# Kernel optimization log

Hardware: AMD Instinct MI355X
Metric: run time of the kernel (lower is better)

## Reference

```python
import jax, jax.numpy as jnp
import numpy as np


def _topk_masked_softmax(attn, k):
    # Keep only the top-k entries per row (last dim), softmax over them.
    _, idx = jax.lax.top_k(attn, k)  # [b, nh, C, k]
    mask = jnp.put_along_axis(
        jnp.zeros(attn.shape, dtype=bool), idx, True, axis=-1, inplace=False
    )
    return jax.nn.softmax(jnp.where(mask, attn, -jnp.inf), axis=-1)


def setup_inputs() -> dict:
    key = jax.random.key(0)
    k0, k1, k2, k3, k4 = jax.random.split(key, 5)
    b, nh, C = 8, 8, 512
    attn = jax.random.normal(k0, (b, nh, C, C), dtype=jnp.float32)
    # In the torch module these are Parameters initialized to 0.2; use random
    # positive scalars of similar scale for a non-degenerate baseline.
    w1 = jax.random.uniform(k1, (1,), dtype=jnp.float32)
    w2 = jax.random.uniform(k2, (1,), dtype=jnp.float32)
    w3 = jax.random.uniform(k3, (1,), dtype=jnp.float32)
    w4 = jax.random.uniform(k4, (1,), dtype=jnp.float32)
    return {"attn": attn, "w1": w1, "w2": w2, "w3": w3, "w4": w4}


def reference(attn, w1, w2, w3, w4):
    C = attn.shape[-1]
    a1 = _topk_masked_softmax(attn, int(C / 2))
    a2 = _topk_masked_softmax(attn, int(C * 2 / 3))
    a3 = _topk_masked_softmax(attn, int(C * 3 / 4))
    a4 = _topk_masked_softmax(attn, int(C * 4 / 5))
    return a1 * w1 + a2 * w2 + a3 * w3 + a4 * w4
```

## Files before the change

kernel.cpp:

```cpp
#include <hip/hip_runtime.h>
#include <math.h>

#define ROW_C 512
#define NBIN 2048
#define NPACK (NBIN / 2)

__global__ __launch_bounds__(256) void topk_ms_kernel(
    const float* __restrict__ attn,
    const float* __restrict__ w1p, const float* __restrict__ w2p,
    const float* __restrict__ w3p, const float* __restrict__ w4p,
    float* __restrict__ out)
{
    __shared__ __align__(16) unsigned hist_all[4][NPACK];

    const int lane = threadIdx.x & 63;
    const int wv   = threadIdx.x >> 6;
    unsigned* h = hist_all[wv];
    int4* hv = (int4*)h;

    const long long row  = (long long)blockIdx.x * 4 + wv;
    const long long base = row * ROW_C + lane * 8;

    const float4 A = *reinterpret_cast<const float4*>(attn + base);
    const float4 B = *reinterpret_cast<const float4*>(attn + base + 4);
    const float orig[8] = {A.x, A.y, A.z, A.w, B.x, B.y, B.z, B.w};

    unsigned key[8];
    int bin[8];
    float eo[8];
    #pragma unroll
    for (int s = 0; s < 8; ++s) {
        const unsigned u = __float_as_uint(orig[s]);
        key[s] = (u & 0x80000000u) ? ~u : (u | 0x80000000u);
        const float y = fminf(fmaxf(orig[s], -3.90625f), 3.90625f) + 12.0f;
        bin[s] = (int)((__float_as_uint(y) >> 12) & 0x7FFu);
        eo[s] = __expf(orig[s]);
    }

    {
        const int4 z = make_int4(0, 0, 0, 0);
        hv[lane] = z; hv[lane + 64] = z; hv[lane + 128] = z; hv[lane + 192] = z;
    }

    #pragma unroll
    for (int s = 0; s < 8; ++s) {
        const int j  = bin[s] >> 1;
        const int ph = j ^ ((j >> 3) & 0x1C);
        atomicAdd(&h[ph], (bin[s] & 1) ? 0x10000u : 1u);
    }

    unsigned ps = 0;
    #pragma unroll
    for (int k = 0; k < 4; ++k) {
        const int b  = 4 * lane + k;
        const int pb = b ^ ((b >> 3) & 7);
        const int4 v = hv[pb];
        ps += (unsigned)v.x + (unsigned)v.y + (unsigned)v.z + (unsigned)v.w;
    }
    const unsigned tot = (ps & 0xFFFFu) + (ps >> 16);

    unsigned incl = tot;
    #pragma unroll
    for (int off = 1; off < 64; off <<= 1) {
        const unsigned t = __shfl_up(incl, off, 64);
        if (lane >= off) incl += t;
    }
    const unsigned excl = incl - tot;

    const unsigned long long Ba = __ballot(incl >= 257u);
    const unsigned long long Bb = __ballot(incl >= 172u);
    const unsigned long long Bc = __ballot(incl >= 129u);
    const unsigned long long Bd = __ballot(incl >= 104u);
    const int l0 = __ffsll(Ba) - 1, l1 = __ffsll(Bb) - 1,
              l2 = __ffsll(Bc) - 1, l3 = __ffsll(Bd) - 1;

    const int lsel = (lane == 0) ? l0 : (lane == 1) ? l1 : (lane == 2) ? l2 : l3;
    const int Tr   = (lane == 0) ? 257 : (lane == 1) ? 172 : (lane == 2) ? 129 : 104;
    const int Kr   = (lane == 0) ? 256 : (lane == 1) ? 341 : (lane == 2) ? 384 : 409;
    const unsigned exl = __shfl(excl, lsel & 63, 64);

    unsigned brR = 0u;
    if (lane < 4) {
        const int Tl = Tr - (int)exl;
        const unsigned T16 = (unsigned)Tl << 16;
        const int jbase = lsel << 4;
        const int xr = ((lsel >> 1) & 7) << 2;
        unsigned w[16];
        #pragma unroll
        for (int q = 0; q < 4; ++q) {
            const int pw = ((jbase + (q << 2)) ^ xr) >> 2;
            const int4 v = hv[pw];
            w[4*q+0] = (unsigned)v.x; w[4*q+1] = (unsigned)v.y;
            w[4*q+2] = (unsigned)v.z; w[4*q+3] = (unsigned)v.w;
        }
        unsigned run = 0, pcap = 0, rcap = 0; int jcap = 0; bool found = false;
        #pragma unroll
        for (int j = 0; j < 16; ++j) {
            const unsigned p = (w[j] + (w[j] << 16)) + (run + (run << 16));
            const bool ge   = (p >= T16);
            const bool take = ge && !found;
            pcap = take ? p   : pcap;
            rcap = take ? run : rcap;
            jcap = take ? j   : jcap;
            found = found || ge;
            run = p >> 16;
        }
        const int  lo   = (int)(pcap & 0xFFFFu);
        const bool ev   = (lo >= Tl);
        const int  bsel = (lsel << 5) + (jcap << 1) + (ev ? 0 : 1);
        const int  locp = ev ? lo : (int)(pcap >> 16);
        const int  prvp = ev ? (int)rcap : lo;
        const int  R    = Kr - 512 + (int)exl + locp;
        const unsigned allin = (prvp == Tl - 1) ? 1u : 0u;
        brR = ((unsigned)bsel << 17) | (allin << 16) | (unsigned)R;
    }

    int br_[4], Rr_[4], al_[4];
    #pragma unroll
    for (int r = 0; r < 4; ++r) {
        const unsigned v = __shfl(brR, r, 64);
        br_[r] = (int)(v >> 17);
        al_[r] = (int)((v >> 16) & 1u);
        Rr_[r] = (int)(v & 0xFFFFu);
    }

    unsigned tk[4]; int need[4], cnteq[4];
    #pragma unroll
    for (int r = 0; r < 4; ++r) {
        tk[r] = 0u; need[r] = 0; cnteq[r] = 0;
        if (!al_[r]) {
            unsigned cm[8];
            #pragma unroll
            for (int s = 0; s < 8; ++s)
                cm[s] = (bin[s] == br_[r]) ? key[s] : 0u;
            int R = Rr_[r];
            unsigned t; int c;
            while (true) {
                unsigned mk = cm[0];
                #pragma unroll
                for (int s = 1; s < 8; ++s) mk = (cm[s] > mk) ? cm[s] : mk;
                #pragma unroll
                for (int off = 32; off >= 1; off >>= 1) {
                    const unsigned o = __shfl_xor(mk, off, 64);
                    mk = (o > mk) ? o : mk;
                }
                t = mk;
                c = 0;
                #pragma unroll
                for (int s = 0; s < 8; ++s)
                    c += (int)__popcll(__ballot(cm[s] == t));
                if (c >= R) break;
                R -= c;
                #pragma unroll
                for (int s = 0; s < 8; ++s)
                    if (cm[s] == t) cm[s] = 0u;
            }
            tk[r] = t; need[r] = R; cnteq[r] = c;
        }
    }

    int fl[8] = {0, 0, 0, 0, 0, 0, 0, 0};
    #pragma unroll
    for (int r = 0; r < 4; ++r) {
        if (al_[r]) {
            const int bb = br_[r];
            #pragma unroll
            for (int s = 0; s < 8; ++s)
                fl[s] |= ((int)(bin[s] >= bb)) << r;
        } else if (need[r] == cnteq[r]) {
            const unsigned t = tk[r];
            #pragma unroll
            for (int s = 0; s < 8; ++s)
                fl[s] |= ((int)(key[s] >= t)) << r;
        } else {
            const unsigned t = tk[r];
            const unsigned long long ltm = (1ull << lane) - 1ull;
            int basec = 0;
            #pragma unroll
            for (int s = 0; s < 8; ++s)
                basec += (int)__popcll(__ballot(key[s] == t) & ltm);
            int own = 0;
            #pragma unroll
            for (int s = 0; s < 8; ++s) {
                const bool eq = (key[s] == t);
                if (key[s] > t || (eq && (basec + own) < need[r]))
                    fl[s] |= (1 << r);
                own += eq ? 1 : 0;
            }
        }
    }

    float z0 = 0.f, z1 = 0.f, z2 = 0.f, z3 = 0.f;
    #pragma unroll
    for (int s = 0; s < 8; ++s) {
        z0 += (fl[s] & 1) ? eo[s] : 0.f;
        z1 += (fl[s] & 2) ? eo[s] : 0.f;
        z2 += (fl[s] & 4) ? eo[s] : 0.f;
        z3 += (fl[s] & 8) ? eo[s] : 0.f;
    }
    #pragma unroll
    for (int off = 32; off >= 1; off >>= 1) {
        z0 += __shfl_xor(z0, off, 64);
        z1 += __shfl_xor(z1, off, 64);
        z2 += __shfl_xor(z2, off, 64);
        z3 += __shfl_xor(z3, off, 64);
    }

    const float wz0 = w1p[0] * __builtin_amdgcn_rcpf(z0);
    const float wz1 = w2p[0] * __builtin_amdgcn_rcpf(z1);
    const float wz2 = w3p[0] * __builtin_amdgcn_rcpf(z2);
    const float wz3 = w4p[0] * __builtin_amdgcn_rcpf(z3);

    float res[8];
    #pragma unroll
    for (int s = 0; s < 8; ++s) {
        float c = 0.f;
        c += (fl[s] & 1) ? wz0 : 0.f;
        c += (fl[s] & 2) ? wz1 : 0.f;
        c += (fl[s] & 4) ? wz2 : 0.f;
        c += (fl[s] & 8) ? wz3 : 0.f;
        res[s] = eo[s] * c;
    }
    *reinterpret_cast<float4*>(out + base)     = make_float4(res[0], res[1], res[2], res[3]);
    *reinterpret_cast<float4*>(out + base + 4) = make_float4(res[4], res[5], res[6], res[7]);
}

extern "C" void kernel_launch(void* const* d_in, const int* in_sizes, int n_in,
                              void* d_out, int out_size, void* d_ws, size_t ws_size,
                              hipStream_t stream) {
    const float* attn = (const float*)d_in[0];
    const float* w1   = (const float*)d_in[1];
    const float* w2   = (const float*)d_in[2];
    const float* w3   = (const float*)d_in[3];
    const float* w4   = (const float*)d_in[4];
    float* out = (float*)d_out;

    int rows = in_sizes[0] / ROW_C;
    int blocks = (rows + 3) / 4;
    topk_ms_kernel<<<blocks, 256, 0, stream>>>(attn, w1, w2, w3, w4, out);
}
```

Before: 136.4 us.

## Parallelize fine-bin search across 16-lane groups and compare floats directly

The bin-level search for each of the four top-k thresholds now runs on 16 lanes per threshold with a shuffle prefix scan, instead of one lane doing a serial 16-word scan. The sortable-integer keys are dropped in favour of comparing float values directly, and clamping uses fmed3. A fast path is added for the common case with no ties at a threshold: membership becomes four nested float comparisons with precomputed cumulative weights instead of building and decoding bit flags. This cuts serial latency and VALU work per wave, at the cost of more code and a divergent branch.

```diff
diff --git a/kernel.cpp b/kernel.cpp
--- a/kernel.cpp
+++ b/kernel.cpp
@@ -23,18 +23,15 @@
 
     const float4 A = *reinterpret_cast<const float4*>(attn + base);
     const float4 B = *reinterpret_cast<const float4*>(attn + base + 4);
-    const float orig[8] = {A.x, A.y, A.z, A.w, B.x, B.y, B.z, B.w};
-
-    unsigned key[8];
+    float x[8] = {A.x, A.y, A.z, A.w, B.x, B.y, B.z, B.w};
+
     int bin[8];
     float eo[8];
     #pragma unroll
     for (int s = 0; s < 8; ++s) {
-        const unsigned u = __float_as_uint(orig[s]);
-        key[s] = (u & 0x80000000u) ? ~u : (u | 0x80000000u);
-        const float y = fminf(fmaxf(orig[s], -3.90625f), 3.90625f) + 12.0f;
+        const float y = __builtin_amdgcn_fmed3f(x[s], -3.90625f, 3.90625f) + 12.0f;
         bin[s] = (int)((__float_as_uint(y) >> 12) & 0x7FFu);
-        eo[s] = __expf(orig[s]);
+        eo[s] = __expf(x[s]);
     }
 
     {
@@ -63,7 +60,7 @@
     #pragma unroll
     for (int off = 1; off < 64; off <<= 1) {
         const unsigned t = __shfl_up(incl, off, 64);
-        if (lane >= off) incl += t;
+        incl += (lane >= off) ? t : 0u;
     }
     const unsigned excl = incl - tot;
 
@@ -74,76 +71,72 @@
     const int l0 = __ffsll(Ba) - 1, l1 = __ffsll(Bb) - 1,
               l2 = __ffsll(Bc) - 1, l3 = __ffsll(Bd) - 1;
 
-    const int lsel = (lane == 0) ? l0 : (lane == 1) ? l1 : (lane == 2) ? l2 : l3;
-    const int Tr   = (lane == 0) ? 257 : (lane == 1) ? 172 : (lane == 2) ? 129 : 104;
-    const int Kr   = (lane == 0) ? 256 : (lane == 1) ? 341 : (lane == 2) ? 384 : 409;
-    const unsigned exl = __shfl(excl, lsel & 63, 64);
-
-    unsigned brR = 0u;
-    if (lane < 4) {
-        const int Tl = Tr - (int)exl;
-        const unsigned T16 = (unsigned)Tl << 16;
-        const int jbase = lsel << 4;
-        const int xr = ((lsel >> 1) & 7) << 2;
-        unsigned w[16];
-        #pragma unroll
-        for (int q = 0; q < 4; ++q) {
-            const int pw = ((jbase + (q << 2)) ^ xr) >> 2;
-            const int4 v = hv[pw];
-            w[4*q+0] = (unsigned)v.x; w[4*q+1] = (unsigned)v.y;
-            w[4*q+2] = (unsigned)v.z; w[4*q+3] = (unsigned)v.w;
-        }
-        unsigned run = 0, pcap = 0, rcap = 0; int jcap = 0; bool found = false;
-        #pragma unroll
-        for (int j = 0; j < 16; ++j) {
-            const unsigned p = (w[j] + (w[j] << 16)) + (run + (run << 16));
-            const bool ge   = (p >= T16);
-            const bool take = ge && !found;
-            pcap = take ? p   : pcap;
-            rcap = take ? run : rcap;
-            jcap = take ? j   : jcap;
-            found = found || ge;
-            run = p >> 16;
-        }
-        const int  lo   = (int)(pcap & 0xFFFFu);
-        const bool ev   = (lo >= Tl);
-        const int  bsel = (lsel << 5) + (jcap << 1) + (ev ? 0 : 1);
-        const int  locp = ev ? lo : (int)(pcap >> 16);
-        const int  prvp = ev ? (int)rcap : lo;
-        const int  R    = Kr - 512 + (int)exl + locp;
-        const unsigned allin = (prvp == Tl - 1) ? 1u : 0u;
-        brR = ((unsigned)bsel << 17) | (allin << 16) | (unsigned)R;
-    }
-
-    int br_[4], Rr_[4], al_[4];
-    #pragma unroll
-    for (int r = 0; r < 4; ++r) {
-        const unsigned v = __shfl(brR, r, 64);
-        br_[r] = (int)(v >> 17);
-        al_[r] = (int)((v >> 16) & 1u);
-        Rr_[r] = (int)(v & 0xFFFFu);
-    }
-
-    unsigned tk[4]; int need[4], cnteq[4];
-    #pragma unroll
-    for (int r = 0; r < 4; ++r) {
-        tk[r] = 0u; need[r] = 0; cnteq[r] = 0;
-        if (!al_[r]) {
-            unsigned cm[8];
+    const int r = lane >> 4;
+    const int i = lane & 15;
+    const int lsel = (r == 0) ? l0 : (r == 1) ? l1 : (r == 2) ? l2 : l3;
+    const int Tr   = (r == 0) ? 257 : (r == 1) ? 172 : (r == 2) ? 129 : 104;
+    const int Kr   = (r == 0) ? 256 : (r == 1) ? 341 : (r == 2) ? 384 : 409;
+    const unsigned exl = __shfl(excl, lsel, 64);
+
+    const int jw = (lsel << 4) + i;
+    const int pw = jw ^ ((jw >> 3) & 0x1C);
+    const unsigned w0 = h[pw];
+    const unsigned q  = w0 + (w0 << 16);
+    const unsigned wt = q >> 16;
+    unsigned sc = wt;
+    #pragma unroll
+    for (int off = 1; off < 16; off <<= 1) {
+        const unsigned t = __shfl_up(sc, off, 64);
+        sc += (i >= off) ? t : 0u;
+    }
+    const unsigned ebase = exl + (sc - wt);
+    const int      phi   = (int)(ebase + wt);
+    const unsigned long long CB = __ballot(phi >= Tr);
+    const int js = __ffs((unsigned)(CB >> (r << 4))) - 1;
+    const unsigned q_w  = __shfl(q, (r << 4) + js, 64);
+    const unsigned eb_w = __shfl(ebase, (r << 4) + js, 64);
+
+    const int  plo  = (int)(eb_w + (q_w & 0xFFFFu));
+    const int  phw  = (int)(eb_w + (q_w >> 16));
+    const bool ev   = (plo >= Tr);
+    const int  bsel = (((lsel << 4) + js) << 1) + (ev ? 0 : 1);
+    const int  locp = ev ? plo : phw;
+    const int  prvp = ev ? (int)eb_w : plo;
+    const int  Rr   = Kr - 512 + locp;
+    const int  alin = (prvp == Tr - 1) ? 1 : 0;
+    float tje = __uint_as_float((unsigned)(bsel + 0x41000) << 12) - 12.0f;
+    tje = (bsel <= 24) ? -__builtin_inff() : tje;
+    const unsigned pk = ((unsigned)bsel << 11) | ((unsigned)alin << 10) | (unsigned)Rr;
+
+    int b_[4], R_[4], al_[4]; float tthr[4];
+    #pragma unroll
+    for (int rr = 0; rr < 4; ++rr) {
+        const unsigned v = __shfl(pk, rr << 4, 64);
+        tthr[rr] = __shfl(tje, rr << 4, 64);
+        b_[rr]  = (int)(v >> 11);
+        al_[rr] = (int)((v >> 10) & 1u);
+        R_[rr]  = (int)(v & 0x3FFu);
+    }
+
+    int needv[4] = {0,0,0,0}, cntv[4] = {0,0,0,0};
+    bool anytb = false;
+    const float NINF = -__builtin_inff();
+    #pragma unroll
+    for (int rr = 0; rr < 4; ++rr) {
+        if (!al_[rr]) {
+            float cm[8];
             #pragma unroll
             for (int s = 0; s < 8; ++s)
-                cm[s] = (bin[s] == br_[r]) ? key[s] : 0u;
-            int R = Rr_[r];
-            unsigned t; int c;
+                cm[s] = (bin[s] == b_[rr]) ? x[s] : NINF;
+            int R = R_[rr];
+            float t; int c;
             while (true) {
-                unsigned mk = cm[0];
-                #pragma unroll
-                for (int s = 1; s < 8; ++s) mk = (cm[s] > mk) ? cm[s] : mk;
-                #pragma unroll
-                for (int off = 32; off >= 1; off >>= 1) {
-                    const unsigned o = __shfl_xor(mk, off, 64);
-                    mk = (o > mk) ? o : mk;
-                }
+                float mk = cm[0];
+                #pragma unroll
+                for (int s = 1; s < 8; ++s) mk = fmaxf(mk, cm[s]);
+                #pragma unroll
+                for (int off = 32; off >= 1; off >>= 1)
+                    mk = fmaxf(mk, __shfl_xor(mk, off, 64));
                 t = mk;
                 c = 0;
                 #pragma unroll
@@ -153,74 +146,99 @@
                 R -= c;
                 #pragma unroll
                 for (int s = 0; s < 8; ++s)
-                    if (cm[s] == t) cm[s] = 0u;
+                    cm[s] = (cm[s] == t) ? NINF : cm[s];
             }
-            tk[r] = t; need[r] = R; cnteq[r] = c;
-        }
-    }
-
-    int fl[8] = {0, 0, 0, 0, 0, 0, 0, 0};
-    #pragma unroll
-    for (int r = 0; r < 4; ++r) {
-        if (al_[r]) {
-            const int bb = br_[r];
-            #pragma unroll
-            for (int s = 0; s < 8; ++s)
-                fl[s] |= ((int)(bin[s] >= bb)) << r;
-        } else if (need[r] == cnteq[r]) {
-            const unsigned t = tk[r];
-            #pragma unroll
-            for (int s = 0; s < 8; ++s)
-                fl[s] |= ((int)(key[s] >= t)) << r;
-        } else {
-            const unsigned t = tk[r];
-            const unsigned long long ltm = (1ull << lane) - 1ull;
-            int basec = 0;
-            #pragma unroll
-            for (int s = 0; s < 8; ++s)
-                basec += (int)__popcll(__ballot(key[s] == t) & ltm);
-            int own = 0;
-            #pragma unroll
-            for (int s = 0; s < 8; ++s) {
-                const bool eq = (key[s] == t);
-                if (key[s] > t || (eq && (basec + own) < need[r]))
-                    fl[s] |= (1 << r);
-                own += eq ? 1 : 0;
+            tthr[rr] = t; needv[rr] = R; cntv[rr] = c;
+            anytb = anytb || (c != R);
+        }
+    }
+
+    float res[8];
+    if (!anytb) {
+        const float t1 = tthr[0], t2 = tthr[1], t3 = tthr[2], t4 = tthr[3];
+        float z0 = 0.f, z1 = 0.f, z2 = 0.f, z3 = 0.f;
+        #pragma unroll
+        for (int s = 0; s < 8; ++s) {
+            z0 += (x[s] >= t1) ? eo[s] : 0.f;
+            z1 += (x[s] >= t2) ? eo[s] : 0.f;
+            z2 += (x[s] >= t3) ? eo[s] : 0.f;
+            z3 += (x[s] >= t4) ? eo[s] : 0.f;
+        }
+        #pragma unroll
+        for (int off = 32; off >= 1; off >>= 1) {
+            z0 += __shfl_xor(z0, off, 64);
+            z1 += __shfl_xor(z1, off, 64);
+            z2 += __shfl_xor(z2, off, 64);
+            z3 += __shfl_xor(z3, off, 64);
+        }
+        const float wz0 = w1p[0] * __builtin_amdgcn_rcpf(z0);
+        const float wz1 = w2p[0] * __builtin_amdgcn_rcpf(z1);
+        const float wz2 = w3p[0] * __builtin_amdgcn_rcpf(z2);
+        const float wz3 = w4p[0] * __builtin_amdgcn_rcpf(z3);
+        const float u4 = wz3, u3 = u4 + wz2, u2 = u3 + wz1, u1 = u2 + wz0;
+        #pragma unroll
+        for (int s = 0; s < 8; ++s) {
+            float c = (x[s] >= t1) ? u1 : u2;
+            c = (x[s] >= t2) ? c : u3;
+            c = (x[s] >= t3) ? c : u4;
+            c = (x[s] >= t4) ? c : 0.f;
+            res[s] = eo[s] * c;
+        }
+    } else {
+        int fl[8] = {0, 0, 0, 0, 0, 0, 0, 0};
+        #pragma unroll
+        for (int rr = 0; rr < 4; ++rr) {
+            const float t = tthr[rr];
+            if (al_[rr] || needv[rr] == cntv[rr]) {
+                #pragma unroll
+                for (int s = 0; s < 8; ++s)
+                    fl[s] |= ((int)(x[s] >= t)) << rr;
+            } else {
+                const unsigned long long ltm = (1ull << lane) - 1ull;
+                int basec = 0;
+                #pragma unroll
+                for (int s = 0; s < 8; ++s)
+                    basec += (int)__popcll(__ballot(x[s] == t) & ltm);
+                int own = 0;
+                #pragma unroll
+                for (int s = 0; s < 8; ++s) {
+                    const bool eq = (x[s] == t);
+                    if (x[s] > t || (eq && (basec + own) < needv[rr]))
+                        fl[s] |= (1 << rr);
+                    own += eq ? 1 : 0;
+                }
             }
         }
-    }
-
-    float z0 = 0.f, z1 = 0.f, z2 = 0.f, z3 = 0.f;
-    #pragma unroll
-    for (int s = 0; s < 8; ++s) {
-        z0 += (fl[s] & 1) ? eo[s] : 0.f;
-        z1 += (fl[s] & 2) ? eo[s] : 0.f;
-        z2 += (fl[s] & 4) ? eo[s] : 0.f;
-        z3 += (fl[s] & 8) ? eo[s] : 0.f;
-    }
-    #pragma unroll
-    for (int off = 32; off >= 1; off >>= 1) {
-        z0 += __shfl_xor(z0, off, 64);
-        z1 += __shfl_xor(z1, off, 64);
-        z2 += __shfl_xor(z2, off, 64);
-        z3 += __shfl_xor(z3, off, 64);
-    }
-
-    const float wz0 = w1p[0] * __builtin_amdgcn_rcpf(z0);
-    const float wz1 = w2p[0] * __builtin_amdgcn_rcpf(z1);
-    const float wz2 = w3p[0] * __builtin_amdgcn_rcpf(z2);
-    const float wz3 = w4p[0] * __builtin_amdgcn_rcpf(z3);
-
-    float res[8];
-    #pragma unroll
-    for (int s = 0; s < 8; ++s) {
-        float c = 0.f;
-        c += (fl[s] & 1) ? wz0 : 0.f;
-        c += (fl[s] & 2) ? wz1 : 0.f;
-        c += (fl[s] & 4) ? wz2 : 0.f;
-        c += (fl[s] & 8) ? wz3 : 0.f;
-        res[s] = eo[s] * c;
-    }
+        float z0 = 0.f, z1 = 0.f, z2 = 0.f, z3 = 0.f;
+        #pragma unroll
+        for (int s = 0; s < 8; ++s) {
+            z0 += (fl[s] & 1) ? eo[s] : 0.f;
+            z1 += (fl[s] & 2) ? eo[s] : 0.f;
+            z2 += (fl[s] & 4) ? eo[s] : 0.f;
+            z3 += (fl[s] & 8) ? eo[s] : 0.f;
+        }
+        #pragma unroll
+        for (int off = 32; off >= 1; off >>= 1) {
+            z0 += __shfl_xor(z0, off, 64);
+            z1 += __shfl_xor(z1, off, 64);
+            z2 += __shfl_xor(z2, off, 64);
+            z3 += __shfl_xor(z3, off, 64);
+        }
+        const float wz0 = w1p[0] * __builtin_amdgcn_rcpf(z0);
+        const float wz1 = w2p[0] * __builtin_amdgcn_rcpf(z1);
+        const float wz2 = w3p[0] * __builtin_amdgcn_rcpf(z2);
+        const float wz3 = w4p[0] * __builtin_amdgcn_rcpf(z3);
+        #pragma unroll
+        for (int s = 0; s < 8; ++s) {
+            float c = 0.f;
+            c += (fl[s] & 1) ? wz0 : 0.f;
+            c += (fl[s] & 2) ? wz1 : 0.f;
+            c += (fl[s] & 4) ? wz2 : 0.f;
+            c += (fl[s] & 8) ? wz3 : 0.f;
+            res[s] = eo[s] * c;
+        }
+    }
+
     *reinterpret_cast<float4*>(out + base)     = make_float4(res[0], res[1], res[2], res[3]);
     *reinterpret_cast<float4*>(out + base + 4) = make_float4(res[4], res[5], res[6], res[7]);
 }
```

After: 128.9 us. -5.5%, faster.
